# Optimization experiments

Measured on AMD Instinct MI355X. Metric: run time of the kernel, lower is better.

## Reference

```python
import jax, jax.numpy as jnp
import numpy as np

HEAD_NUM = 16
EMBED = 1024
B, T = 2, 2048


def setup_inputs() -> dict:
    key = jax.random.key(0)
    k1, k2, k3 = jax.random.split(key, 3)
    x = jax.random.normal(k1, (B, T, EMBED), dtype=jnp.float32)
    # torch Linear weights: [out_features, in_features]; scaled like default init
    w_qkv = jax.random.normal(k2, (3 * EMBED, EMBED), dtype=jnp.float32) / np.sqrt(EMBED)
    w_out = jax.random.normal(k3, (EMBED, EMBED), dtype=jnp.float32) / np.sqrt(EMBED)
    return {"x": x, "w_qkv": w_qkv, "w_out": w_out}


def reference(x, w_qkv, w_out):
    b, t, e = x.shape
    h = HEAD_NUM
    d = e // h
    dk = d ** 0.5  # NOTE: original MULTIPLIES scores by sqrt(head_dim)
    qkv = x @ w_qkv.T  # [b, t, 3e]
    # einops 'b t (d k h) -> k b h t d' with k=3: split order is (d, 3, h)
    qkv = qkv.reshape(b, t, d, 3, h)
    qkv = jnp.transpose(qkv, (3, 0, 4, 1, 2))  # [3, b, h, t, d]
    q, k, v = qkv[0], qkv[1], qkv[2]
    energy = jnp.einsum('bhid,bhjd->bhij', q, k) * dk  # [b, h, t, t]
    attn = jax.nn.softmax(energy, axis=-1)
    out = jnp.einsum('bhij,bhjd->bhid', attn, v)  # [b, h, t, d]
    out = jnp.transpose(out, (0, 2, 1, 3)).reshape(b, t, e)  # b t (h d)
    return out @ w_out.T
```

## Files before the change

kernel.cpp:

```cpp
#include <hip/hip_runtime.h>
#include <hip/hip_bf16.h>

typedef _Float16 f16x8 __attribute__((ext_vector_type(8)));
typedef unsigned short u16x8 __attribute__((ext_vector_type(8)));
typedef unsigned short u16x4 __attribute__((ext_vector_type(4)));
typedef float f32x4 __attribute__((ext_vector_type(4)));

static constexpr int Bn = 2;
static constexpr int Tn = 2048;
static constexpr int En = 1024;
static constexpr int Hn = 16;
static constexpr int Dn = 64;
#define LOG2E 1.44269504088896340736f

static constexpr int TS = 136;
static constexpr int PS = 40;

__device__ __forceinline__ unsigned short f2h(float x) {
  _Float16 h = (_Float16)x;
  return __builtin_bit_cast(unsigned short, h);
}
__device__ __forceinline__ float h2f(unsigned short u) {
  return (float)__builtin_bit_cast(_Float16, u);
}
__device__ __forceinline__ f16x8 ldh8(const unsigned short* p) {
  return __builtin_bit_cast(f16x8, *reinterpret_cast<const u16x8*>(p));
}
__device__ __forceinline__ unsigned int pk2(float a, float b) {
  return __builtin_bit_cast(unsigned int, __builtin_amdgcn_cvt_pkrtz(a, b));
}
__device__ __forceinline__ void gld16(const void* g, void* l) {
  __builtin_amdgcn_global_load_lds(
      (__attribute__((address_space(1))) void*)(const_cast<void*>(g)),
      (__attribute__((address_space(3))) void*)(l), 16, 0, 0);
}

__global__ __launch_bounds__(256) void split_f32_f16(
    const float* __restrict__ src, unsigned short* __restrict__ hi,
    unsigned short* __restrict__ lo)
{
  const int i = (blockIdx.x * 256 + threadIdx.x) * 4;
  const float4 v = *reinterpret_cast<const float4*>(src + i);
  ushort4 h, l;
  h.x = f2h(v.x); l.x = f2h(v.x - h2f(h.x));
  h.y = f2h(v.y); l.y = f2h(v.y - h2f(h.y));
  h.z = f2h(v.z); l.z = f2h(v.z - h2f(h.z));
  h.w = f2h(v.w); l.w = f2h(v.w - h2f(h.w));
  *reinterpret_cast<ushort4*>(hi + i) = h;
  *reinterpret_cast<ushort4*>(lo + i) = l;
}

__global__ __launch_bounds__(256) void cvt_f32_f16(
    const float* __restrict__ src, unsigned short* __restrict__ dst)
{
  const int i = (blockIdx.x * 256 + threadIdx.x) * 4;
  const float4 v = *reinterpret_cast<const float4*>(src + i);
  ushort4 u;
  u.x = f2h(v.x); u.y = f2h(v.y); u.z = f2h(v.z); u.w = f2h(v.w);
  *reinterpret_cast<ushort4*>(dst + i) = u;
}

__global__ __launch_bounds__(256) void gemm_qkv(
    const unsigned short* __restrict__ xh, const unsigned short* __restrict__ xl,
    const unsigned short* __restrict__ wf,
    unsigned short* __restrict__ Qf, unsigned short* __restrict__ Kf,
    unsigned short* __restrict__ Vf, int M, int K)
{
  __shared__ unsigned short smem[128 * TS];
  unsigned short* shAh = smem;
  unsigned short* shAl = smem + 4096;
  unsigned short* shB = smem + 8192;

  const int tid = threadIdx.x;
  const int w = tid >> 6, L = tid & 63, qd = L >> 4, lr = L & 15;
  const int m0 = blockIdx.y * 128;
  const int kk = blockIdx.x >> 3;
  const int hh0 = (blockIdx.x & 7) * 2;
  const int wm = (w >> 1) * 64, wn = (w & 1) * 64;

  f32x4 acc[4][4] = {};

  for (int k0 = 0; k0 < K; k0 += 32) {
#pragma unroll
    for (int p = 0; p < 2; ++p) {
      const int c = p * 256 + tid;
      const int row = c >> 2, slot = c & 3;
      const int dd = row & 63, hl = row >> 6;
      const int nB = dd * 48 + kk * 16 + hh0 + hl;
      const size_t aoff = (size_t)(m0 + row) * K + k0 + slot * 8;
      const size_t boff = (size_t)nB * K + k0 + slot * 8;
      const int base = (p * 4 + w) * 512;
      gld16(xh + aoff, &shAh[base]);
      gld16(wf + boff, &shB[base]);
      if (kk < 2) gld16(xl + aoff, &shAl[base]);
    }
    __syncthreads();

    f16x8 afh[4], bf[4];
#pragma unroll
    for (int mt = 0; mt < 4; ++mt)
      afh[mt] = ldh8(&shAh[(wm + mt * 16 + lr) * 32 + qd * 8]);
#pragma unroll
    for (int nt = 0; nt < 4; ++nt)
      bf[nt] = ldh8(&shB[(wn + nt * 16 + lr) * 32 + qd * 8]);
    if (kk < 2) {
      f16x8 afl[4];
#pragma unroll
      for (int mt = 0; mt < 4; ++mt)
        afl[mt] = ldh8(&shAl[(wm + mt * 16 + lr) * 32 + qd * 8]);
#pragma unroll
      for (int mt = 0; mt < 4; ++mt)
#pragma unroll
        for (int nt = 0; nt < 4; ++nt) {
          acc[mt][nt] = __builtin_amdgcn_mfma_f32_16x16x32_f16(afh[mt], bf[nt], acc[mt][nt], 0, 0, 0);
          acc[mt][nt] = __builtin_amdgcn_mfma_f32_16x16x32_f16(afl[mt], bf[nt], acc[mt][nt], 0, 0, 0);
        }
    } else {
#pragma unroll
      for (int mt = 0; mt < 4; ++mt)
#pragma unroll
        for (int nt = 0; nt < 4; ++nt)
          acc[mt][nt] = __builtin_amdgcn_mfma_f32_16x16x32_f16(afh[mt], bf[nt], acc[mt][nt], 0, 0, 0);
    }
    __syncthreads();
  }

  const int b = m0 >> 11;
  const int t0 = m0 & (Tn - 1);
  const float qscale = (kk == 0) ? 8.0f * LOG2E : 1.0f;
#pragma unroll
  for (int mt = 0; mt < 4; ++mt)
#pragma unroll
    for (int nt = 0; nt < 4; ++nt)
#pragma unroll
      for (int r = 0; r < 4; ++r) {
        const int ml = wm + mt * 16 + qd * 4 + r;
        const int cl = wn + nt * 16 + lr;
        smem[ml * TS + cl] = f2h(acc[mt][nt][r] * qscale);
      }
  __syncthreads();

  unsigned short* dst = (kk == 0) ? Qf : (kk == 1) ? Kf : Vf;
  if (kk < 2) {
#pragma unroll
    for (int p = 0; p < 8; ++p) {
      const int s = p * 256 + tid;
      const int tl = s >> 4, sub = s & 15;
      const int hl = sub >> 3, oct = sub & 7;
      const u16x8 v = *reinterpret_cast<const u16x8*>(&smem[tl * TS + hl * 64 + oct * 8]);
      *reinterpret_cast<u16x8*>(
          dst + ((size_t)(b * Hn + hh0 + hl) * Tn + t0 + tl) * Dn + oct * 8) = v;
    }
  } else {
#pragma unroll
    for (int p = 0; p < 8; ++p) {
      const int s = p * 256 + tid;
      const int cl = s >> 4, oct = s & 15;
      const int hl = cl >> 6, dd = cl & 63;
      u16x8 v;
#pragma unroll
      for (int j = 0; j < 8; ++j) v[j] = smem[(oct * 8 + j) * TS + cl];
      *reinterpret_cast<u16x8*>(
          dst + ((size_t)((b * Hn + hh0 + hl) * Dn + dd)) * Tn + t0 + oct * 8) = v;
    }
  }
}

__global__ __launch_bounds__(256, 2) void attn_kernel(
    const unsigned short* __restrict__ Qf, const unsigned short* __restrict__ Kf,
    const unsigned short* __restrict__ Vf, unsigned short* __restrict__ AOf)
{
  __shared__ unsigned short shK[2 * 128 * 32];
  __shared__ unsigned short shV[4 * 64 * 32];
  __shared__ unsigned short shP[4 * 16 * PS];
  const int tid = threadIdx.x;
  const int w = tid >> 6, L = tid & 63, qd = L >> 4, lr = L & 15;
  const int q0 = blockIdx.x * 64;
  const int bh = blockIdx.y;
  unsigned short* myP = &shP[w * 16 * PS];

  f16x8 aq[2];
  {
    const size_t qoff = ((size_t)bh * Tn + q0 + w * 16 + lr) * Dn;
    aq[0] = ldh8(Qf + qoff + qd * 8);
    aq[1] = ldh8(Qf + qoff + 32 + qd * 8);
  }
  f16x8 ones;
#pragma unroll
  for (int j = 0; j < 8; ++j) ones[j] = (_Float16)1.0f;

  f32x4 oacc[4] = {};
  float mrow = -1e30f, lsum = 0.f;

  for (int j0 = 0; j0 < Tn; j0 += 128) {
#pragma unroll
    for (int p = 0; p < 4; ++p) {
      const int kc = p >> 1, half = p & 1;
      const int row = half * 64 + (tid >> 2);
      const int slot = tid & 3;
      gld16(Kf + ((size_t)bh * Tn + j0 + row) * Dn + kc * 32 + slot * 8,
            &shK[kc * 4096 + (half * 64 + w * 16) * 32]);
    }
#pragma unroll
    for (int p = 0; p < 4; ++p) {
      const int dd = tid >> 2, slot = tid & 3;
      gld16(Vf + ((size_t)bh * Dn + dd) * Tn + j0 + p * 32 + slot * 8,
            &shV[p * 2048 + (w * 16) * 32]);
    }
    __syncthreads();

    f32x4 s2[8];
#pragma unroll
    for (int ct = 0; ct < 8; ++ct) {
      const int rk = ct * 16 + lr;
      s2[ct] = f32x4{0.f, 0.f, 0.f, 0.f};
#pragma unroll
      for (int kc = 0; kc < 2; ++kc) {
        const f16x8 bk = ldh8(&shK[kc * 4096 + rk * 32 + qd * 8]);
        s2[ct] = __builtin_amdgcn_mfma_f32_16x16x32_f16(bk, aq[kc], s2[ct], 0, 0, 0);
      }
    }

    float tm = s2[0][0];
#pragma unroll
    for (int ct = 0; ct < 8; ++ct)
#pragma unroll
      for (int r = 0; r < 4; ++r) tm = fmaxf(tm, s2[ct][r]);
    tm = fmaxf(tm, __shfl_xor(tm, 16, 64));
    tm = fmaxf(tm, __shfl_xor(tm, 32, 64));
    const float mn = fmaxf(mrow, tm);
    const float alpha = exp2f(mrow - mn);
    mrow = mn;
#pragma unroll
    for (int ct = 0; ct < 8; ++ct)
#pragma unroll
      for (int r = 0; r < 4; ++r)
        s2[ct][r] = exp2f(s2[ct][r] - mrow);
#pragma unroll
    for (int nt = 0; nt < 4; ++nt)
#pragma unroll
      for (int r = 0; r < 4; ++r) oacc[nt][r] *= alpha;

    f32x4 sacc = {};
#pragma unroll
    for (int kcv = 0; kcv < 4; ++kcv) {
#pragma unroll
      for (int c2 = 0; c2 < 2; ++c2) {
        const int ct = kcv * 2 + c2;
        uint2 d2;
        d2.x = pk2(s2[ct][0], s2[ct][1]);
        d2.y = pk2(s2[ct][2], s2[ct][3]);
        *reinterpret_cast<uint2*>(&myP[lr * PS + c2 * 16 + qd * 4]) = d2;
      }
      const f16x8 pa = ldh8(&myP[lr * PS + qd * 8]);
#pragma unroll
      for (int nt = 0; nt < 4; ++nt) {
        const f16x8 bv = ldh8(&shV[kcv * 2048 + (nt * 16 + lr) * 32 + qd * 8]);
        oacc[nt] = __builtin_amdgcn_mfma_f32_16x16x32_f16(bv, pa, oacc[nt], 0, 0, 0);
      }
      sacc = __builtin_amdgcn_mfma_f32_16x16x32_f16(ones, pa, sacc, 0, 0, 0);
    }
    lsum = lsum * alpha + sacc[0];
    __syncthreads();
  }

  const int b = bh >> 4, h = bh & 15;
  const float inv = 1.0f / lsum;
  const int q = q0 + w * 16 + lr;
#pragma unroll
  for (int nt = 0; nt < 4; ++nt) {
    unsigned short o[4];
#pragma unroll
    for (int r = 0; r < 4; ++r) o[r] = f2h(oacc[nt][r] * inv);
    const int col = h * 64 + nt * 16 + qd * 4;
    *reinterpret_cast<u16x4*>(&AOf[((size_t)b * Tn + q) * En + col]) =
        u16x4{o[0], o[1], o[2], o[3]};
  }
}

__global__ __launch_bounds__(256) void gemm_out(
    const unsigned short* __restrict__ A, const unsigned short* __restrict__ Bm,
    float* __restrict__ C, int M, int N, int K)
{
  __shared__ unsigned short shA[128 * 32];
  __shared__ unsigned short shB[128 * 32];
  const int tid = threadIdx.x;
  const int w = tid >> 6, L = tid & 63, qd = L >> 4, lr = L & 15;
  const int m0 = blockIdx.y * 128;
  const int n0 = blockIdx.x * 128;
  const int wm = (w >> 1) * 64, wn = (w & 1) * 64;

  f32x4 acc[4][4] = {};

  for (int k0 = 0; k0 < K; k0 += 32) {
#pragma unroll
    for (int p = 0; p < 2; ++p) {
      const int c = p * 256 + tid;
      const int row = c >> 2, slot = c & 3;
      const int base = (p * 4 + w) * 512;
      gld16(A + (size_t)(m0 + row) * K + k0 + slot * 8, &shA[base]);
      gld16(Bm + (size_t)(n0 + row) * K + k0 + slot * 8, &shB[base]);
    }
    __syncthreads();

    f16x8 af[4], bf[4];
#pragma unroll
    for (int mt = 0; mt < 4; ++mt)
      af[mt] = ldh8(&shA[(wm + mt * 16 + lr) * 32 + qd * 8]);
#pragma unroll
    for (int nt = 0; nt < 4; ++nt)
      bf[nt] = ldh8(&shB[(wn + nt * 16 + lr) * 32 + qd * 8]);
#pragma unroll
    for (int mt = 0; mt < 4; ++mt)
#pragma unroll
      for (int nt = 0; nt < 4; ++nt)
        acc[mt][nt] = __builtin_amdgcn_mfma_f32_16x16x32_f16(af[mt], bf[nt], acc[mt][nt], 0, 0, 0);
    __syncthreads();
  }

#pragma unroll
  for (int mt = 0; mt < 4; ++mt)
#pragma unroll
    for (int nt = 0; nt < 4; ++nt)
#pragma unroll
      for (int r = 0; r < 4; ++r) {
        const int m = m0 + wm + mt * 16 + qd * 4 + r;
        const int n = n0 + wn + nt * 16 + lr;
        C[(size_t)m * N + n] = acc[mt][nt][r];
      }
}

extern "C" void kernel_launch(void* const* d_in, const int* in_sizes, int n_in,
                              void* d_out, int out_size, void* d_ws, size_t ws_size,
                              hipStream_t stream) {
  (void)in_sizes; (void)n_in; (void)out_size; (void)ws_size;
  const float* x = (const float*)d_in[0];
  const float* wqkv = (const float*)d_in[1];
  const float* wout = (const float*)d_in[2];
  float* out = (float*)d_out;

  const size_t elems = (size_t)Bn * Hn * Tn * Dn;
  unsigned short* Qf = (unsigned short*)d_ws;
  unsigned short* Kf = Qf + elems;
  unsigned short* Vf = Kf + elems;
  unsigned short* AOf = Vf + elems;
  unsigned short* wf = AOf + elems;
  unsigned short* wof = wf + (size_t)3 * En * En;

  unsigned short* xh = (unsigned short*)d_out;
  unsigned short* xl = xh + elems;

  const int M = Bn * Tn;
  dim3 blk(256);
  split_f32_f16<<<dim3((int)(elems / 1024)), blk, 0, stream>>>(x, xh, xl);
  cvt_f32_f16<<<dim3(3 * En * En / 1024), blk, 0, stream>>>(wqkv, wf);
  cvt_f32_f16<<<dim3(En * En / 1024), blk, 0, stream>>>(wout, wof);
  gemm_qkv<<<dim3(24, M / 128), blk, 0, stream>>>(
      xh, xl, wf, Qf, Kf, Vf, M, En);
  attn_kernel<<<dim3(Tn / 64, Bn * Hn), blk, 0, stream>>>(Qf, Kf, Vf, AOf);
  gemm_out<<<dim3(En / 128, M / 128), blk, 0, stream>>>(
      AOf, wof, out, M, En, En);
}
```

Baseline: 266.7 us.

## Double-buffer shared memory tiles in QKV GEMM to overlap loads with MFMA

The QKV projection GEMM now uses two shared-memory buffers. The next K-slice is issued with async global-to-LDS loads while MFMAs run on the current slice, and the per-iteration address math is hoisted out of the loop. This is meant to hide global load latency that previously stalled each iteration behind a barrier. In exchange LDS use doubles to 48KB, which may lower occupancy, and correctness depends on the async loads being complete by the end-of-iteration barrier.

```diff
diff --git a/kernel.cpp b/kernel.cpp
--- a/kernel.cpp
+++ b/kernel.cpp
@@ -66,10 +66,7 @@
     unsigned short* __restrict__ Qf, unsigned short* __restrict__ Kf,
     unsigned short* __restrict__ Vf, int M, int K)
 {
-  __shared__ unsigned short smem[128 * TS];
-  unsigned short* shAh = smem;
-  unsigned short* shAl = smem + 4096;
-  unsigned short* shB = smem + 8192;
+  __shared__ unsigned short smem[2 * 12288];
 
   const int tid = threadIdx.x;
   const int w = tid >> 6, L = tid & 63, qd = L >> 4, lr = L & 15;
@@ -78,36 +75,53 @@
   const int hh0 = (blockIdx.x & 7) * 2;
   const int wm = (w >> 1) * 64, wn = (w & 1) * 64;
 
+  size_t aoffs[2], boffs[2];
+  int lbase[2];
+#pragma unroll
+  for (int p = 0; p < 2; ++p) {
+    const int c = p * 256 + tid;
+    const int row = c >> 2, slot = c & 3;
+    const int dd = row & 63, hl = row >> 6;
+    aoffs[p] = (size_t)(m0 + row) * K + slot * 8;
+    boffs[p] = (size_t)(dd * 48 + kk * 16 + hh0 + hl) * K + slot * 8;
+    lbase[p] = (p * 4 + w) * 512;
+  }
+
   f32x4 acc[4][4] = {};
 
+#pragma unroll
+  for (int p = 0; p < 2; ++p) {
+    gld16(xh + aoffs[p], &smem[lbase[p]]);
+    gld16(wf + boffs[p], &smem[8192 + lbase[p]]);
+    if (kk < 2) gld16(xl + aoffs[p], &smem[4096 + lbase[p]]);
+  }
+  __syncthreads();
+
+  int buf = 0;
   for (int k0 = 0; k0 < K; k0 += 32) {
-#pragma unroll
-    for (int p = 0; p < 2; ++p) {
-      const int c = p * 256 + tid;
-      const int row = c >> 2, slot = c & 3;
-      const int dd = row & 63, hl = row >> 6;
-      const int nB = dd * 48 + kk * 16 + hh0 + hl;
-      const size_t aoff = (size_t)(m0 + row) * K + k0 + slot * 8;
-      const size_t boff = (size_t)nB * K + k0 + slot * 8;
-      const int base = (p * 4 + w) * 512;
-      gld16(xh + aoff, &shAh[base]);
-      gld16(wf + boff, &shB[base]);
-      if (kk < 2) gld16(xl + aoff, &shAl[base]);
-    }
-    __syncthreads();
-
+    if (k0 + 32 < K) {
+      const int nb = (buf ^ 1) * 12288;
+#pragma unroll
+      for (int p = 0; p < 2; ++p) {
+        gld16(xh + aoffs[p] + k0 + 32, &smem[nb + lbase[p]]);
+        gld16(wf + boffs[p] + k0 + 32, &smem[nb + 8192 + lbase[p]]);
+        if (kk < 2) gld16(xl + aoffs[p] + k0 + 32, &smem[nb + 4096 + lbase[p]]);
+      }
+    }
+
+    const int cb = buf * 12288;
     f16x8 afh[4], bf[4];
 #pragma unroll
     for (int mt = 0; mt < 4; ++mt)
-      afh[mt] = ldh8(&shAh[(wm + mt * 16 + lr) * 32 + qd * 8]);
-#pragma unroll
-    for (int nt = 0; nt < 4; ++nt)
-      bf[nt] = ldh8(&shB[(wn + nt * 16 + lr) * 32 + qd * 8]);
+      afh[mt] = ldh8(&smem[cb + (wm + mt * 16 + lr) * 32 + qd * 8]);
+#pragma unroll
+    for (int nt = 0; nt < 4; ++nt)
+      bf[nt] = ldh8(&smem[cb + 8192 + (wn + nt * 16 + lr) * 32 + qd * 8]);
     if (kk < 2) {
       f16x8 afl[4];
 #pragma unroll
       for (int mt = 0; mt < 4; ++mt)
-        afl[mt] = ldh8(&shAl[(wm + mt * 16 + lr) * 32 + qd * 8]);
+        afl[mt] = ldh8(&smem[cb + 4096 + (wm + mt * 16 + lr) * 32 + qd * 8]);
 #pragma unroll
       for (int mt = 0; mt < 4; ++mt)
 #pragma unroll
@@ -123,6 +137,7 @@
           acc[mt][nt] = __builtin_amdgcn_mfma_f32_16x16x32_f16(afh[mt], bf[nt], acc[mt][nt], 0, 0, 0);
     }
     __syncthreads();
+    buf ^= 1;
   }
 
   const int b = m0 >> 11;
```

Result: faster. 245.7 us (-7.9%).
